# Kernel optimization log

Measured on AMD Instinct MI355X. Metric: run time of the kernel, lower is better.

Reference implementation:

```python
import jax, jax.numpy as jnp
import numpy as np

P = 12           # AR order == number of rollout steps
N = 2048         # input_size (nodes)
B = 128          # batch
C = 1            # channels (only channel 0 used)


def setup_inputs() -> dict:
    key = jax.random.key(0)
    kx, kw = jax.random.split(key)
    x = jax.random.normal(kx, (B, N, C, P), dtype=jnp.float32)
    W = jax.random.normal(kw, (P, N, N), dtype=jnp.float32)
    return {"x": x, "W": W}


def reference(x, W):
    # x: [B, N, C, L]; take channel 0 and transpose -> [B, L(=p), N]
    xt = jnp.transpose(x[:, :, 0, :], (0, 2, 1))

    def step(xc, _):
        # einsum('ijk,bik->bij') followed by sum over i fuses to 'ijk,bik->bj'
        y = jnp.einsum('ijk,bik->bj', W, xc)              # [B, N]
        xc = jnp.concatenate([xc[:, 1:, :], y[:, None, :]], axis=1)  # shift window
        return xc, y

    _, ys = jax.lax.scan(step, xt, None, length=12)       # ys: [12, B, N]
    return jnp.transpose(ys, (1, 2, 0))                   # [B, N, 12]
```

## Files before the change

kernel.cpp:

```cpp
#include <hip/hip_runtime.h>
#include <stdint.h>


typedef _Float16 f16x8 __attribute__((ext_vector_type(8)));
typedef float    f32x4 __attribute__((ext_vector_type(4)));

#define B_ 128
#define N_ 2048
#define P_ 12
#define K_ (P_*N_)
#define NT 16
#define NKP (K_/64)

#define WPK_BYTES    ((size_t)NT*NKP*16384)
#define H_SLOT_BYTES ((size_t)B_*N_*2)
#define H_BYTES      (23*H_SLOT_BYTES)
#define CH_BYTES     ((size_t)B_*N_*2)
#define PF_BYTES     (78*CH_BYTES)
#define PFB_BYTES    (44*CH_BYTES)
#define WS_NEEDED    (WPK_BYTES + H_BYTES + PF_BYTES + PFB_BYTES)

__device__ __constant__ int E_TAB[11] = {7, 13, 18, 24, 29, 35, 40, 46, 51, 57, 62};

__device__ __forceinline__ float pow2f(int e) {
    return __uint_as_float((uint32_t)(127 + e) << 23);
}

union F16x8 { _Float16 h[8]; uint4 q; };
union F16x4v { _Float16 h[4]; uint2 q; };

__device__ __forceinline__ uint32_t h_off(int slot, int b, int k) {
    return (uint32_t)slot * (uint32_t)H_SLOT_BYTES
         + (uint32_t)(k >> 5) * 8192u + (uint32_t)(((k >> 3) & 3) << 11)
         + (uint32_t)(b << 4) + (uint32_t)((k & 7) << 1);
}
__device__ __forceinline__ size_t w_tile_base(int nt, int pk) {
    return ((size_t)nt * NKP + (size_t)pk) * 16384;
}

__global__ void prep_all(const float* __restrict__ x, const float* __restrict__ W,
                         char* __restrict__ Wp, char* __restrict__ H)
{
    __shared__ float tile[128][68];
    int bid = blockIdx.x, t = threadIdx.x;
    if (bid < 128) {
        int tg = bid * 256 + t;
        int b = tg >> 8;
        int n0 = (tg & 255) << 3;
        const float4* s4 = (const float4*)(x + ((size_t)b * N_ + n0) * P_);
        float4 tmp[24];
        #pragma unroll
        for (int i2 = 0; i2 < 24; ++i2) tmp[i2] = s4[i2];
        #pragma unroll
        for (int p = 0; p < 12; ++p) {
            F16x8 o;
            #pragma unroll
            for (int q = 0; q < 8; ++q) {
                int fi = q * 12 + p;
                float4 blk = tmp[fi >> 2];
                float f = ((fi & 3) == 0) ? blk.x : ((fi & 3) == 1) ? blk.y : ((fi & 3) == 2) ? blk.z : blk.w;
                o.h[q] = (_Float16)f;
            }
            *(uint4*)(H + h_off(p, b, n0)) = o.q;
        }
        return;
    }
    int u = bid - 128;
    int nt = u / NKP, pk = u % NKP;
    int i  = pk >> 5;
    int k0 = (pk & 31) << 6;
    int j0 = nt << 7;
    #pragma unroll
    for (int pass = 0; pass < 8; ++pass) {
        int jl = pass * 16 + (t >> 4);
        int kq = (t & 15) * 4;
        float4 v = *(const float4*)(W + ((size_t)i * N_ + (j0 + jl)) * N_ + k0 + kq);
        tile[jl][kq + 0] = v.x; tile[jl][kq + 1] = v.y;
        tile[jl][kq + 2] = v.z; tile[jl][kq + 3] = v.w;
    }
    __syncthreads();
    int ksub = t >> 7, c = t & 127;
    char* base = Wp + w_tile_base(nt, pk) + (ksub << 13);
    #pragma unroll
    for (int ko = 0; ko < 4; ++ko) {
        F16x8 o;
        #pragma unroll
        for (int q = 0; q < 8; ++q) o.h[q] = (_Float16)tile[c][ksub * 32 + ko * 8 + q];
        uint32_t off = (uint32_t)((c << 6) + (ko << 4)) ^ (uint32_t)((c & 7) << 4);
        *(uint4*)(base + off) = o.q;
    }
}

__device__ __forceinline__ void gemm_body(
        const char* __restrict__ Wp, const char* __restrict__ H,
        _Float16* __restrict__ part, char* ldsB,
        int nt, int pk0, int slot, int k0, int nph)
{
    const int tid  = threadIdx.x;
    const int lane = tid & 63;
    const int wv   = tid >> 6;
    const int wr   = wv >> 1;
    const int wc   = wv & 1;
    const int l15  = lane & 15;
    const int ko   = lane >> 4;
    const int jbase = (nt << 7) + (wc << 6) + l15;

    uint32_t boff[4];
    #pragma unroll
    for (int nf = 0; nf < 4; ++nf) {
        int c = (wc << 6) + (nf << 4) + l15;
        boff[nf] = (uint32_t)((c << 6) + (ko << 4)) ^ (uint32_t)((c & 7) << 4);
    }

    auto stage = [&](int buf, int ph) {
        const char* src = Wp + w_tile_base(nt, pk0 + ph);
        #pragma unroll
        for (int j = 0; j < 4; ++j) {
            uint32_t o = (uint32_t)(j << 12) + (uint32_t)(tid << 4);
            __builtin_amdgcn_global_load_lds(
                (const __attribute__((address_space(1))) void*)(src + o),
                (__attribute__((address_space(3))) void*)(ldsB + buf * 16384 + (j << 12) + (wv << 10)), 16, 0, 0);
        }
    };
    auto loadA = [&](int ph, f16x8 a[2][4]) {
        #pragma unroll
        for (int ksub = 0; ksub < 2; ++ksub) {
            int k = k0 + (ph << 6) + (ksub << 5);
            const char* sb = H + (size_t)slot * H_SLOT_BYTES
                           + (uint32_t)((k >> 5) << 13) + (uint32_t)(ko << 11);
            #pragma unroll
            for (int m = 0; m < 4; ++m) {
                int brow = (wr << 6) + (m << 4) + l15;
                a[ksub][m] = *(const f16x8*)(sb + (brow << 4));
            }
        }
    };

    f32x4 acc[4][4];
    #pragma unroll
    for (int m = 0; m < 4; ++m)
        #pragma unroll
        for (int n = 0; n < 4; ++n) acc[m][n] = (f32x4){0.f, 0.f, 0.f, 0.f};

    f16x8 a[2][4];
    loadA(0, a);
    stage(0, 0);
    __syncthreads();

    #pragma unroll 1
    for (int ph = 0; ph < nph; ++ph) {
        if (ph + 1 < nph) stage((ph & 1) ^ 1, ph + 1);
        const char* lb = ldsB + (ph & 1) * 16384;
        f16x8 bf[2][4];
        #pragma unroll
        for (int ksub = 0; ksub < 2; ++ksub)
            #pragma unroll
            for (int nf = 0; nf < 4; ++nf)
                bf[ksub][nf] = *(const f16x8*)(lb + (ksub << 13) + boff[nf]);
        f16x8 an[2][4];
        if (ph + 1 < nph) loadA(ph + 1, an);
        #pragma unroll
        for (int ksub = 0; ksub < 2; ++ksub)
            #pragma unroll
            for (int m = 0; m < 4; ++m)
                #pragma unroll
                for (int nf = 0; nf < 4; ++nf)
                    acc[m][nf] = __builtin_amdgcn_mfma_f32_16x16x32_f16(a[ksub][m], bf[ksub][nf], acc[m][nf], 0, 0, 0);
        #pragma unroll
        for (int ksub = 0; ksub < 2; ++ksub)
            #pragma unroll
            for (int m = 0; m < 4; ++m) a[ksub][m] = an[ksub][m];
        __syncthreads();
    }

    const int r0 = (lane >> 4) << 2;
    _Float16* pb = part + ((size_t)((wr << 6) + r0)) * N_ + jbase;
    #pragma unroll
    for (int m = 0; m < 4; ++m)
        #pragma unroll
        for (int n = 0; n < 4; ++n)
            #pragma unroll
            for (int r = 0; r < 4; ++r)
                pb[(size_t)(m * 16 + r) * N_ + n * 16] = (_Float16)acc[m][n][r];
}

__global__ __launch_bounds__(256, 2) void gemm_F(
        const char* __restrict__ Wp, const char* __restrict__ H,
        _Float16* __restrict__ pF)
{
    __shared__ alignas(16) char ldsB[2 * 16384];
    int bid = blockIdx.x;
    int bucket = bid / 96;
    int w = bid % 96;
    int m  = w >> 3;
    int g  = bucket * 8 + (w & 7);
    int j  = g >> 4;
    int nt = g & 15;
    int s  = j + m;
    if (s > 11) return;
    int t = m;
    int idx = t * 12 - t * (t - 1) / 2 + j;
    gemm_body(Wp, H, pF + (size_t)idx * (CH_BYTES / 2), ldsB,
              nt, j * 32, s, 0, 32);
}

__global__ __launch_bounds__(256, 2) void gemm_FB(
        const char* __restrict__ Wp, const char* __restrict__ H,
        _Float16* __restrict__ pFB, int t)
{
    __shared__ alignas(16) char ldsB[2 * 16384];
    int c = blockIdx.x >> 4, nt = blockIdx.x & 15;
    int j = c >> 2, sub = c & 3;
    int i = 12 - t + j;
    gemm_body(Wp, H, pFB + (size_t)c * (CH_BYTES / 2), ldsB,
              nt, i * 32 + sub * 8, 12 + j, sub * 512, 8);
}

__global__ void reduce_step(const _Float16* __restrict__ pF, const _Float16* __restrict__ pFB,
                            float* __restrict__ out, char* __restrict__ H, int t)
{
    int tid = blockIdx.x * 256 + threadIdx.x;
    int b = tid >> 9;
    int n0 = (tid & 511) << 2;
    const size_t eo = (size_t)b * N_ + n0;
    float s0 = 0.f, s1 = 0.f, s2 = 0.f, s3 = 0.f;
    int baseT = t * 12 - t * (t - 1) / 2;
    int nF = 12 - t;
    #pragma unroll 4
    for (int f = 0; f < nF; ++f) {
        F16x4v p;
        p.q = *(const uint2*)(pF + (size_t)(baseT + f) * (CH_BYTES / 2) + eo);
        s0 += (float)p.h[0]; s1 += (float)p.h[1];
        s2 += (float)p.h[2]; s3 += (float)p.h[3];
    }
    #pragma unroll 4
    for (int c = 0; c < 4 * t; ++c) {
        float sc = pow2f(E_TAB[c >> 2]);
        F16x4v p;
        p.q = *(const uint2*)(pFB + (size_t)c * (CH_BYTES / 2) + eo);
        s0 += (float)p.h[0] * sc; s1 += (float)p.h[1] * sc;
        s2 += (float)p.h[2] * sc; s3 += (float)p.h[3] * sc;
    }
    float* ob = out + eo * P_ + t;
    ob[0 * P_] = s0; ob[1 * P_] = s1; ob[2 * P_] = s2; ob[3 * P_] = s3;
    if (t < 11) {
        float ds = pow2f(-E_TAB[t]);
        F16x4v o;
        o.h[0] = (_Float16)(s0 * ds); o.h[1] = (_Float16)(s1 * ds);
        o.h[2] = (_Float16)(s2 * ds); o.h[3] = (_Float16)(s3 * ds);
        *(uint2*)(H + h_off(12 + t, b, n0)) = o.q;
    }
}

__global__ void naive_step(const float* __restrict__ x, const float* __restrict__ W,
                           float* __restrict__ out, int t)
{
    int tid = blockIdx.x * 256 + threadIdx.x;
    int b = tid >> 11;
    int j = tid & (N_ - 1);
    float acc = 0.f;
    for (int i = 0; i < 12; ++i) {
        int g = t + i;
        const float* src = (g < 12) ? (x   + (size_t)b * (N_ * 12) + g)
                                    : (out + (size_t)b * (N_ * 12) + (g - 12));
        const float* wr = W + ((size_t)i * N_ + j) * N_;
        for (int k = 0; k < N_; ++k)
            acc += wr[k] * src[(size_t)k * 12];
    }
    out[((size_t)b * N_ + j) * 12 + t] = acc;
}

extern "C" void kernel_launch(void* const* d_in, const int* in_sizes, int n_in,
                              void* d_out, int out_size, void* d_ws, size_t ws_size,
                              hipStream_t stream)
{
    const float* x = (const float*)d_in[0];
    const float* W = (const float*)d_in[1];
    float* out = (float*)d_out;

    if (ws_size < WS_NEEDED) {
        for (int t = 0; t < 12; ++t)
            naive_step<<<1024, 256, 0, stream>>>(x, W, out, t);
        return;
    }

    char* Wp = (char*)d_ws;
    char* H  = Wp + WPK_BYTES;
    _Float16* pF  = (_Float16*)(H + H_BYTES);
    _Float16* pFB = (_Float16*)(H + H_BYTES + PF_BYTES);

    prep_all<<<6272, 256, 0, stream>>>(x, W, Wp, H);
    gemm_F<<<2304, 256, 0, stream>>>(Wp, H, pF);
    reduce_step<<<256, 256, 0, stream>>>(pF, pFB, out, H, 0);
    for (int t = 1; t < 12; ++t) {
        gemm_FB<<<64 * t, 256, 0, stream>>>(Wp, H, pFB, t);
        reduce_step<<<256, 256, 0, stream>>>(pF, pFB, out, H, t);
    }
}
```

Baseline: 492.4 us.

## Stage activation tiles through LDS with swizzled layout alongside weight tiles

The activation operand (H) is now stored in a swizzled, row-major-by-batch layout and staged into LDS with async global_load_lds, next to the weight tile, in place of the direct per-lane global loads into registers. The K step per phase is halved to 32 so the combined A+B double buffer still fits in 32 KB, and the phase counts are doubled to match. Launch bounds rise from 2 to 4 blocks per SM, aiming for higher occupancy now that the register prefetch of A is gone. The cost is twice as many phases, and so twice as many barriers, plus extra LDS traffic for A.

```diff
diff --git a/kernel.cpp b/kernel.cpp
--- a/kernel.cpp
+++ b/kernel.cpp
@@ -30,9 +30,8 @@
 union F16x4v { _Float16 h[4]; uint2 q; };
 
 __device__ __forceinline__ uint32_t h_off(int slot, int b, int k) {
-    return (uint32_t)slot * (uint32_t)H_SLOT_BYTES
-         + (uint32_t)(k >> 5) * 8192u + (uint32_t)(((k >> 3) & 3) << 11)
-         + (uint32_t)(b << 4) + (uint32_t)((k & 7) << 1);
+    uint32_t t = (uint32_t)((b << 6) + ((k & 31) << 1)) ^ (uint32_t)((b & 7) << 4);
+    return (uint32_t)slot * (uint32_t)H_SLOT_BYTES + (uint32_t)(k >> 5) * 8192u + t;
 }
 __device__ __forceinline__ size_t w_tile_base(int nt, int pk) {
     return ((size_t)nt * NKP + (size_t)pk) * 16384;
@@ -93,7 +92,7 @@
 
 __device__ __forceinline__ void gemm_body(
         const char* __restrict__ Wp, const char* __restrict__ H,
-        _Float16* __restrict__ part, char* ldsB,
+        _Float16* __restrict__ part, char* ldsAB,
         int nt, int pk0, int slot, int k0, int nph)
 {
     const int tid  = threadIdx.x;
@@ -105,7 +104,12 @@
     const int ko   = lane >> 4;
     const int jbase = (nt << 7) + (wc << 6) + l15;
 
-    uint32_t boff[4];
+    uint32_t aoff[4], boff[4];
+    #pragma unroll
+    for (int m = 0; m < 4; ++m) {
+        int row = (wr << 6) + (m << 4) + l15;
+        aoff[m] = (uint32_t)((row << 6) + (ko << 4)) ^ (uint32_t)((row & 7) << 4);
+    }
     #pragma unroll
     for (int nf = 0; nf < 4; ++nf) {
         int c = (wc << 6) + (nf << 4) + l15;
@@ -113,28 +117,21 @@
     }
 
     auto stage = [&](int buf, int ph) {
-        const char* src = Wp + w_tile_base(nt, pk0 + ph);
-        #pragma unroll
-        for (int j = 0; j < 4; ++j) {
+        int k = k0 + (ph << 5);
+        const char* sA = H + (size_t)slot * H_SLOT_BYTES + (uint32_t)((k >> 5) << 13);
+        const char* sB = Wp + w_tile_base(nt, pk0 + (ph >> 1)) + (uint32_t)((ph & 1) << 13);
+        #pragma unroll
+        for (int j = 0; j < 2; ++j) {
             uint32_t o = (uint32_t)(j << 12) + (uint32_t)(tid << 4);
+            uint32_t d = (uint32_t)(j << 12) + (uint32_t)(wv << 10);
             __builtin_amdgcn_global_load_lds(
-                (const __attribute__((address_space(1))) void*)(src + o),
-                (__attribute__((address_space(3))) void*)(ldsB + buf * 16384 + (j << 12) + (wv << 10)), 16, 0, 0);
+                (const __attribute__((address_space(1))) void*)(sA + o),
+                (__attribute__((address_space(3))) void*)(ldsAB + buf * 16384 + d), 16, 0, 0);
+            __builtin_amdgcn_global_load_lds(
+                (const __attribute__((address_space(1))) void*)(sB + o),
+                (__attribute__((address_space(3))) void*)(ldsAB + buf * 16384 + 8192 + d), 16, 0, 0);
         }
     };
-    auto loadA = [&](int ph, f16x8 a[2][4]) {
-        #pragma unroll
-        for (int ksub = 0; ksub < 2; ++ksub) {
-            int k = k0 + (ph << 6) + (ksub << 5);
-            const char* sb = H + (size_t)slot * H_SLOT_BYTES
-                           + (uint32_t)((k >> 5) << 13) + (uint32_t)(ko << 11);
-            #pragma unroll
-            for (int m = 0; m < 4; ++m) {
-                int brow = (wr << 6) + (m << 4) + l15;
-                a[ksub][m] = *(const f16x8*)(sb + (brow << 4));
-            }
-        }
-    };
 
     f32x4 acc[4][4];
     #pragma unroll
@@ -142,34 +139,24 @@
         #pragma unroll
         for (int n = 0; n < 4; ++n) acc[m][n] = (f32x4){0.f, 0.f, 0.f, 0.f};
 
-    f16x8 a[2][4];
-    loadA(0, a);
     stage(0, 0);
     __syncthreads();
 
     #pragma unroll 1
     for (int ph = 0; ph < nph; ++ph) {
         if (ph + 1 < nph) stage((ph & 1) ^ 1, ph + 1);
-        const char* lb = ldsB + (ph & 1) * 16384;
-        f16x8 bf[2][4];
-        #pragma unroll
-        for (int ksub = 0; ksub < 2; ++ksub)
+        const char* lA = ldsAB + (ph & 1) * 16384;
+        const char* lB = lA + 8192;
+        f16x8 ah[4], bf[4];
+        #pragma unroll
+        for (int m = 0; m < 4; ++m) ah[m] = *(const f16x8*)(lA + aoff[m]);
+        #pragma unroll
+        for (int nf = 0; nf < 4; ++nf) bf[nf] = *(const f16x8*)(lB + boff[nf]);
+        #pragma unroll
+        for (int m = 0; m < 4; ++m)
             #pragma unroll
             for (int nf = 0; nf < 4; ++nf)
-                bf[ksub][nf] = *(const f16x8*)(lb + (ksub << 13) + boff[nf]);
-        f16x8 an[2][4];
-        if (ph + 1 < nph) loadA(ph + 1, an);
-        #pragma unroll
-        for (int ksub = 0; ksub < 2; ++ksub)
-            #pragma unroll
-            for (int m = 0; m < 4; ++m)
-                #pragma unroll
-                for (int nf = 0; nf < 4; ++nf)
-                    acc[m][nf] = __builtin_amdgcn_mfma_f32_16x16x32_f16(a[ksub][m], bf[ksub][nf], acc[m][nf], 0, 0, 0);
-        #pragma unroll
-        for (int ksub = 0; ksub < 2; ++ksub)
-            #pragma unroll
-            for (int m = 0; m < 4; ++m) a[ksub][m] = an[ksub][m];
+                acc[m][nf] = __builtin_amdgcn_mfma_f32_16x16x32_f16(ah[m], bf[nf], acc[m][nf], 0, 0, 0);
         __syncthreads();
     }
 
@@ -184,11 +171,11 @@
                 pb[(size_t)(m * 16 + r) * N_ + n * 16] = (_Float16)acc[m][n][r];
 }
 
-__global__ __launch_bounds__(256, 2) void gemm_F(
+__global__ __launch_bounds__(256, 4) void gemm_F(
         const char* __restrict__ Wp, const char* __restrict__ H,
         _Float16* __restrict__ pF)
 {
-    __shared__ alignas(16) char ldsB[2 * 16384];
+    __shared__ alignas(16) char ldsAB[2 * 16384];
     int bid = blockIdx.x;
     int bucket = bid / 96;
     int w = bid % 96;
@@ -200,20 +187,20 @@
     if (s > 11) return;
     int t = m;
     int idx = t * 12 - t * (t - 1) / 2 + j;
-    gemm_body(Wp, H, pF + (size_t)idx * (CH_BYTES / 2), ldsB,
-              nt, j * 32, s, 0, 32);
-}
-
-__global__ __launch_bounds__(256, 2) void gemm_FB(
+    gemm_body(Wp, H, pF + (size_t)idx * (CH_BYTES / 2), ldsAB,
+              nt, j * 32, s, 0, 64);
+}
+
+__global__ __launch_bounds__(256, 4) void gemm_FB(
         const char* __restrict__ Wp, const char* __restrict__ H,
         _Float16* __restrict__ pFB, int t)
 {
-    __shared__ alignas(16) char ldsB[2 * 16384];
+    __shared__ alignas(16) char ldsAB[2 * 16384];
     int c = blockIdx.x >> 4, nt = blockIdx.x & 15;
     int j = c >> 2, sub = c & 3;
     int i = 12 - t + j;
-    gemm_body(Wp, H, pFB + (size_t)c * (CH_BYTES / 2), ldsB,
-              nt, i * 32 + sub * 8, 12 + j, sub * 512, 8);
+    gemm_body(Wp, H, pFB + (size_t)c * (CH_BYTES / 2), ldsAB,
+              nt, i * 32 + sub * 8, 12 + j, sub * 512, 16);
 }
 
 __global__ void reduce_step(const _Float16* __restrict__ pF, const _Float16* __restrict__ pFB,
```

Result: faster. 458.3 us (-6.9%).
